# Kernel tuning notes

Hardware: AMD Instinct MI355X
Metric: run time of the kernel (lower is better)

Reference implementation:

```python
import jax, jax.numpy as jnp
import numpy as np

N = 4096          # n_nodes
M = 8192          # m_nodes (= 2*N, required by block structure)
D = 128           # in_dim == hidden_dim (conv1 is reapplied to its own output)
H = 128
NUM_ITERS = 3


def setup_inputs() -> dict:
    key = jax.random.key(0)
    ks = jax.random.split(key, 6)
    X = jax.random.normal(ks[0], (N, D), dtype=jnp.float32)
    R = jax.random.uniform(ks[1], (N, N), dtype=jnp.float32)
    A = 0.5 * (R + R.T)  # symmetric, strictly positive connectivity matrix
    # upsample MLP: Linear(n_nodes -> m_nodes - n_nodes), torch weight layout [out, in]
    W_up = jax.random.normal(ks[2], (M - N, N), dtype=jnp.float32) * 0.02
    b_up = jnp.zeros((M - N,), dtype=jnp.float32)
    # GCNConv linear weights stored [in, out]
    W1 = jax.random.normal(ks[3], (D, H), dtype=jnp.float32) * 0.05
    b1 = jnp.zeros((H,), dtype=jnp.float32)
    W2 = jax.random.normal(ks[4], (H, H), dtype=jnp.float32) * 0.05
    b2 = jnp.zeros((H,), dtype=jnp.float32)
    return dict(X=X, A=A, W_up=W_up, b_up=b_up, W1=W1, b1=b1, W2=W2, b2=b2)


def _gcn(Adj, X, W, b):
    # PyG GCNConv on a fully dense, strictly-positive weighted graph:
    # every diagonal entry is nonzero, so add_remaining_self_loops is a no-op and
    # out = D^{-1/2} A D^{-1/2} (X W) + b  exactly.
    deg = Adj.sum(axis=0)                         # [m] column degree
    dinv = jnp.where(deg > 0, jax.lax.rsqrt(deg), 0.0)
    An = Adj * dinv[:, None] * dinv[None, :]      # symmetric normalization
    return An @ (X @ W) + b


def reference(X, A, W_up, b_up, W1, b1, W2, b2):
    # new_nodes = upsample_mlp(X.T).T  -> [M-N, D]
    new_nodes = (X.T @ W_up.T + b_up).T
    Xu = jnp.concatenate([X, new_nodes], axis=0)  # [M, D]
    # block adjacency: [[A, A.T], [A, sigmoid(new @ new.T)]]
    Adj = jnp.block([[A, A.T],
                     [A, jax.nn.sigmoid(new_nodes @ new_nodes.T)]])  # [M, M]
    A_out = Adj
    for _ in range(NUM_ITERS):
        Xu = jax.nn.relu(_gcn(Adj, Xu, W1, b1))
        Adj = jax.nn.sigmoid(Xu @ Xu.T)           # mid-loop adjacency rebuild
        Xu = jax.nn.relu(_gcn(Adj, Xu, W2, b2))
        A_out = jax.nn.sigmoid(Xu @ Xu.T)
        # NOTE: edge_index for the next conv1 is NOT rebuilt from A_out in the
        # original (only after conv1), so Adj carries the mid-loop matrix.
    return A_out
```

## Files before the change

kernel.cpp:

```cpp
#include <hip/hip_runtime.h>
#include <hip/hip_bf16.h>


#define N_NODES 4096
#define M_NODES 8192
#define DIM 128
#define SLICE_ELEMS ((size_t)M_NODES * DIM)

typedef __attribute__((ext_vector_type(4))) float f32x4;
typedef __attribute__((ext_vector_type(8))) short bf16x8;

__device__ __forceinline__ unsigned short f2bf(float f) {
  union { float f; unsigned u; } v; v.f = f;
  unsigned r = v.u + 0x7fffu + ((v.u >> 16) & 1u);
  return (unsigned short)(r >> 16);
}

__device__ __forceinline__ void gld16(unsigned short* lds, const unsigned short* g) {
  __builtin_amdgcn_global_load_lds(
      (const __attribute__((address_space(1))) unsigned int*)g,
      (__attribute__((address_space(3))) unsigned int*)lds, 16, 0, 0);
}

__device__ __forceinline__ float sigmoidf_(float x) { return 1.0f / (1.0f + __expf(-x)); }


__global__ void cast_x_kernel(const float* __restrict__ X, unsigned short* __restrict__ Xu,
                              unsigned short* __restrict__ XT,
                              float* __restrict__ colsumA) {
  int idx = blockIdx.x * 256 + threadIdx.x;
  if (idx < N_NODES) colsumA[idx] = 0.f;
  int i = idx >> 7, c = idx & 127;
  unsigned short b = f2bf(X[idx]);
  Xu[idx] = b;
  XT[(size_t)c * N_NODES + i] = b;
}

__global__ void cast_wt2_kernel(const float* __restrict__ W1, const float* __restrict__ W2,
                                unsigned short* __restrict__ WT1,
                                unsigned short* __restrict__ WT2) {
  int idx = blockIdx.x * 256 + threadIdx.x;
  const float* W = idx < 16384 ? W1 : W2;
  unsigned short* WT = idx < 16384 ? WT1 : WT2;
  int j = idx & 16383;
  int k = j >> 7, c = j & 127;
  WT[c * DIM + k] = f2bf(W[j]);
}

__global__ void cast_a_kernel(const float* __restrict__ A, unsigned short* __restrict__ Adj,
                              float* __restrict__ colsumA) {
  int c = blockIdx.x * 256 + threadIdx.x;
  int r0 = blockIdx.y * 128;
  int tm = r0 >> 7;
  int kc = c >> 10, st = (c & 1023) >> 5, e = c & 31;
  size_t a1 = ((size_t)(tm)      * 8 + kc)     * 131072 + (size_t)st * 4096 + e;
  size_t a2 = ((size_t)(tm)      * 8 + 4 + kc) * 131072 + (size_t)st * 4096 + e;
  size_t a3 = ((size_t)(tm + 32) * 8 + kc)     * 131072 + (size_t)st * 4096 + e;
  float s = 0.f;
  for (int r = 0; r < 128; ++r) {
    float a = A[(size_t)(r0 + r) * N_NODES + c];
    unsigned short b = f2bf(a);
    Adj[a1 + r * 32] = b; Adj[a2 + r * 32] = b; Adj[a3 + r * 32] = b;
    s += a;
  }
  atomicAdd(&colsumA[c], s);
}

__global__ void init_deg_kernel(const float* __restrict__ colsumA, float* __restrict__ deg) {
  int i = blockIdx.x * 256 + threadIdx.x;
  deg[i] = (i < N_NODES) ? 2.0f * colsumA[i] : colsumA[i - N_NODES];
}


__global__ __launch_bounds__(256, 2)
void agg128_kernel(const unsigned short* __restrict__ At,
                   const unsigned short* __restrict__ BT, long ldb,
                   float* __restrict__ accBase, int kIters) {
  __shared__ __align__(16) unsigned short smem[32768];
  const int t = threadIdx.x, w = t >> 6, lane = t & 63;
  const int q = lane >> 4, l15 = lane & 15;
  const int xk = l15 & 7;
  const int tm = blockIdx.x;
  const int sg0 = blockIdx.y * (kIters * 2);
  const size_t kbase = (size_t)sg0 * 32;

  auto STAGE = [&](int s, int b) {
    unsigned short* la = smem + b * 16384;
    unsigned short* lb = la + 8192;
#pragma unroll
    for (int j = 0; j < 4; ++j) {
      int ch = j * 256 + t;
      int row = ch >> 3, phys = ch & 7;
      int c = phys ^ (row & 7);
      int sg = sg0 + 2 * s + (c >> 2);
      gld16(&la[ch * 8],
            &At[((size_t)tm * 8 + (sg >> 5)) * 131072 + (size_t)(sg & 31) * 4096 +
                row * 32 + (c & 3) * 8]);
      gld16(&lb[ch * 8], &BT[(size_t)row * ldb + kbase + s * 64 + c * 8]);
    }
  };

  f32x4 acc[2][8];
#pragma unroll
  for (int a = 0; a < 2; ++a)
#pragma unroll
    for (int b = 0; b < 8; ++b) acc[a][b] = (f32x4)0.f;

  STAGE(0, 0);

  for (int s = 0; s < kIters; ++s) {
    if (s + 1 < kIters) {
      STAGE(s + 1, (s + 1) & 1);
      asm volatile("s_waitcnt vmcnt(8)" ::: "memory");
    } else {
      asm volatile("s_waitcnt vmcnt(0)" ::: "memory");
    }
    __builtin_amdgcn_s_barrier();
    __builtin_amdgcn_sched_barrier(0);

    const unsigned short* la = smem + (s & 1) * 16384;
    const unsigned short* lb = la + 8192;
#pragma unroll
    for (int kk = 0; kk < 2; ++kk) {
      bf16x8 a0 = *(const bf16x8*)&la[(w * 32 + l15) * 64 + (((kk << 2) + q) ^ xk) * 8];
      bf16x8 a1 = *(const bf16x8*)&la[(w * 32 + 16 + l15) * 64 + (((kk << 2) + q) ^ xk) * 8];
#pragma unroll
      for (int nt = 0; nt < 8; ++nt) {
        bf16x8 b = *(const bf16x8*)&lb[(nt * 16 + l15) * 64 + (((kk << 2) + q) ^ xk) * 8];
        acc[0][nt] = __builtin_amdgcn_mfma_f32_16x16x32_bf16(a0, b, acc[0][nt], 0, 0, 0);
        acc[1][nt] = __builtin_amdgcn_mfma_f32_16x16x32_bf16(a1, b, acc[1][nt], 0, 0, 0);
      }
    }
    __builtin_amdgcn_sched_barrier(0);
    __builtin_amdgcn_s_barrier();
    __builtin_amdgcn_sched_barrier(0);
  }
  float* ct = accBase + (size_t)blockIdx.y * SLICE_ELEMS + (size_t)blockIdx.x * 16384;
#pragma unroll
  for (int mt = 0; mt < 2; ++mt)
#pragma unroll
    for (int nt = 0; nt < 8; ++nt)
      *(f32x4*)&ct[((w * 16 + mt * 8 + nt) * 256) + (q * 16 + l15) * 4] = acc[mt][nt];
}


__global__ __launch_bounds__(256)
void up_agg_f32(const float* __restrict__ Wup, const unsigned short* __restrict__ BT,
                float* __restrict__ accBase) {
  __shared__ __align__(16) unsigned short smem[6144];
  unsigned short* la = smem;
  unsigned short* lb = smem + 2048;
  const int t = threadIdx.x, w = t >> 6, lane = t & 63;
  const int q = lane >> 4, l15 = lane & 15;
  const int r0 = blockIdx.x * 64;
  const int k0 = blockIdx.y * 512;
  const int arow = t >> 2, achk = t & 3;

  f32x4 acc[8];
#pragma unroll
  for (int b = 0; b < 8; ++b) acc[b] = (f32x4)0.f;

  for (int s = 0; s < 16; ++s) {
    int kb = k0 + s * 32;
    __syncthreads();
    gld16(&lb[t * 8],        &BT[(size_t)arow * N_NODES + kb + achk * 8]);
    gld16(&lb[2048 + t * 8], &BT[(size_t)(64 + arow) * N_NODES + kb + achk * 8]);
    const float* ap = &Wup[(size_t)(r0 + (t >> 2)) * N_NODES + kb + (t & 3) * 8];
    float4 v0 = *(const float4*)ap;
    float4 v1 = *(const float4*)(ap + 4);
    ushort4 o0, o1;
    o0.x = f2bf(v0.x); o0.y = f2bf(v0.y); o0.z = f2bf(v0.z); o0.w = f2bf(v0.w);
    o1.x = f2bf(v1.x); o1.y = f2bf(v1.y); o1.z = f2bf(v1.z); o1.w = f2bf(v1.w);
    *(ushort4*)&la[t * 8] = o0;
    *(ushort4*)&la[t * 8 + 4] = o1;
    __syncthreads();

    bf16x8 a0 = *(const bf16x8*)&la[(w * 16 + l15) * 32 + q * 8];
#pragma unroll
    for (int nt = 0; nt < 8; ++nt) {
      bf16x8 b = *(const bf16x8*)&lb[(nt * 16 + l15) * 32 + q * 8];
      acc[nt] = __builtin_amdgcn_mfma_f32_16x16x32_bf16(a0, b, acc[nt], 0, 0, 0);
    }
  }
  float* ct = accBase + (size_t)blockIdx.y * SLICE_ELEMS + (size_t)blockIdx.x * 8192;
#pragma unroll
  for (int nt = 0; nt < 8; ++nt)
    *(f32x4*)&ct[((w * 8 + nt) * 256) + (q * 16 + l15) * 4] = acc[nt];
}

__global__ void reduce64_kernel(const float* __restrict__ acc,
                                unsigned short* __restrict__ dst,
                                const float* __restrict__ bias_row,
                                const float* __restrict__ bias_col,
                                const float* __restrict__ deg, int mode, int nSlices) {
  int p = blockIdx.x * 256 + threadIdx.x;
  float s = 0.f;
  for (int sp = 0; sp < nSlices; ++sp) s += acc[(size_t)sp * SLICE_ELEMS + p];
  int row, col;
  float v;
  if (mode == 0) {
    int tile = p >> 13, r = p & 8191;
    int grp = r >> 8;
    int w = grp >> 3, nt = grp & 7;
    int r2 = r & 255;
    int i = r2 & 3, ql = r2 >> 2;
    row = tile * 64 + w * 16 + (ql >> 4) * 4 + i;
    col = nt * 16 + (ql & 15);
    v = s + bias_row[row];
  } else {
    int tile = p >> 14, r = p & 16383;
    int grp = r >> 8;
    int w = grp >> 4, mt = (grp >> 3) & 1, nt = grp & 7;
    int r2 = r & 255;
    int i = r2 & 3, ql = r2 >> 2;
    row = tile * 128 + w * 32 + mt * 16 + (ql >> 4) * 4 + i;
    col = nt * 16 + (ql & 15);
    float d = deg[row];
    float dv = d > 0.f ? rsqrtf(d) : 0.f;
    v = fmaxf(dv * s + bias_col[col], 0.f);
  }
  dst[(size_t)row * DIM + col] = f2bf(v);
}


template <int MODE>
__global__ __launch_bounds__(256)
void rebuild_kernel(const unsigned short* __restrict__ XA,
                    const unsigned short* __restrict__ XB,
                    void* __restrict__ out, long p1 ,
                    long col0, float* __restrict__ deg, int nB) {
  __shared__ __align__(16) unsigned short smem[34816];
  __shared__ float lcol[128];
  __shared__ float lrow[128];
  unsigned short* lA = smem;
  unsigned short* lB = smem + 16384;
  const int t = threadIdx.x, w = t >> 6, lane = t & 63;
  const int q = lane >> 4, l15 = lane & 15;
  const int sx = (l15 >> 1) & 3;

  int rem = blockIdx.x, bi = 0;
  while (rem >= nB - bi) { rem -= nB - bi; ++bi; }
  const int bj = bi + rem;
  const int i0 = bi * 128, j0 = bj * 128;
  const bool offdiag = (bi != bj);

  const int srow = t >> 2;
  const int xchk = (t & 3) ^ ((t >> 3) & 3);
#pragma unroll
  for (int kk = 0; kk < 4; ++kk)
#pragma unroll
    for (int h = 0; h < 2; ++h) {
      gld16(&lA[kk * 4096 + h * 2048 + t * 8],
            &XA[(size_t)(i0 + h * 64 + srow) * DIM + kk * 32 + xchk * 8]);
      gld16(&lB[kk * 4096 + h * 2048 + t * 8],
            &XB[(size_t)(j0 + h * 64 + srow) * DIM + kk * 32 + xchk * 8]);
    }
  if (MODE == 0 && t < 128) { lcol[t] = 0.f; lrow[t] = 0.f; }
  __syncthreads();

  f32x4 acc[2][8];
#pragma unroll
  for (int a = 0; a < 2; ++a)
#pragma unroll
    for (int b = 0; b < 8; ++b) acc[a][b] = (f32x4)0.f;

#pragma unroll
  for (int kk = 0; kk < 4; ++kk) {
    bf16x8 a0 = *(const bf16x8*)&lA[kk * 4096 + (w * 32 + l15) * 32 + ((q ^ sx)) * 8];
    bf16x8 a1 = *(const bf16x8*)&lA[kk * 4096 + (w * 32 + 16 + l15) * 32 + ((q ^ sx)) * 8];
#pragma unroll
    for (int nt = 0; nt < 8; ++nt) {
      bf16x8 b = *(const bf16x8*)&lB[kk * 4096 + (nt * 16 + l15) * 32 + ((q ^ sx)) * 8];
      acc[0][nt] = __builtin_amdgcn_mfma_f32_16x16x32_bf16(a0, b, acc[0][nt], 0, 0, 0);
      acc[1][nt] = __builtin_amdgcn_mfma_f32_16x16x32_bf16(a1, b, acc[1][nt], 0, 0, 0);
    }
  }
  __syncthreads();

  if (MODE == 0) {
    unsigned short* lC  = smem;
    unsigned short* lCt = smem + 17408;
    float rs[2][4] = {{0.f, 0.f, 0.f, 0.f}, {0.f, 0.f, 0.f, 0.f}};
#pragma unroll
    for (int mt = 0; mt < 2; ++mt)
#pragma unroll
      for (int nt = 0; nt < 8; ++nt) {
        float cs = 0.f;
#pragma unroll
        for (int i = 0; i < 4; ++i) {
          float sv = sigmoidf_(acc[mt][nt][i]);
          cs += sv;
          unsigned short hb = f2bf(sv);
          int row = w * 32 + mt * 16 + q * 4 + i, colL = nt * 16 + l15;
          lC[row * 136 + colL] = hb;
          if (offdiag) { lCt[colL * 136 + row] = hb; rs[mt][i] += sv; }
        }
        cs += __shfl_xor(cs, 16);
        cs += __shfl_xor(cs, 32);
        if (lane < 16) atomicAdd(&lcol[nt * 16 + lane], cs);
      }
    if (offdiag) {
#pragma unroll
      for (int mt = 0; mt < 2; ++mt)
#pragma unroll
        for (int i = 0; i < 4; ++i) {
          float v = rs[mt][i];
          v += __shfl_xor(v, 1); v += __shfl_xor(v, 2);
          v += __shfl_xor(v, 4); v += __shfl_xor(v, 8);
          if (l15 == 0) atomicAdd(&lrow[w * 32 + mt * 16 + q * 4 + i], v);
        }
    }
    __syncthreads();
    unsigned short* og = (unsigned short*)out;
    {
      const long rowbase = p1 + i0, colbase = col0 + j0;
      const size_t tb = ((size_t)(rowbase >> 7) * 8 + (colbase >> 10)) * 131072;
      const int stb = (int)((colbase & 1023) >> 5);
#pragma unroll
      for (int cc = 0; cc < 8; ++cc) {
        int ch = t + cc * 256;
        int row = ch >> 4, c16 = ch & 15;
        *(bf16x8*)&og[tb + (size_t)(stb + (c16 >> 2)) * 4096 + row * 32 + (c16 & 3) * 8] =
            *(const bf16x8*)&lC[row * 136 + c16 * 8];
      }
    }
    if (offdiag) {
      const long rowbase = p1 + j0, colbase = col0 + i0;
      const size_t tb = ((size_t)(rowbase >> 7) * 8 + (colbase >> 10)) * 131072;
      const int stb = (int)((colbase & 1023) >> 5);
#pragma unroll
      for (int cc = 0; cc < 8; ++cc) {
        int ch = t + cc * 256;
        int row = ch >> 4, c16 = ch & 15;
        *(bf16x8*)&og[tb + (size_t)(stb + (c16 >> 2)) * 4096 + row * 32 + (c16 & 3) * 8] =
            *(const bf16x8*)&lCt[row * 136 + c16 * 8];
      }
    }
    if (t < 128) atomicAdd(&deg[col0 + j0 + t], lcol[t]);
    if (offdiag && t < 128) atomicAdd(&deg[col0 + i0 + t], lrow[t]);
  } else {
    float* og = (float*)out;
    float* lCf = (float*)smem;
#pragma unroll
    for (int mt = 0; mt < 2; ++mt)
#pragma unroll
      for (int nt = 0; nt < 8; ++nt)
#pragma unroll
        for (int i = 0; i < 4; ++i) acc[mt][nt][i] = sigmoidf_(acc[mt][nt][i]);
#pragma unroll
    for (int h2 = 0; h2 < 2; ++h2) {
      __syncthreads();
      if ((w >> 1) == h2) {
#pragma unroll
        for (int mt = 0; mt < 2; ++mt)
#pragma unroll
          for (int nt = 0; nt < 8; ++nt)
#pragma unroll
            for (int i = 0; i < 4; ++i)
              lCf[((w & 1) * 32 + mt * 16 + q * 4 + i) * 132 + nt * 16 + l15] =
                  acc[mt][nt][i];
      }
      __syncthreads();
#pragma unroll
      for (int j = 0; j < 8; ++j) {
        int ch = t + j * 256;
        int r64 = ch >> 5, c4 = (ch & 31) * 4;
        *(f32x4*)&og[(size_t)(i0 + h2 * 64 + r64) * p1 + j0 + c4] =
            *(const f32x4*)&lCf[r64 * 132 + c4];
      }
    }
    if (offdiag) {
#pragma unroll
      for (int h2 = 0; h2 < 2; ++h2) {
        __syncthreads();
#pragma unroll
        for (int mt = 0; mt < 2; ++mt)
#pragma unroll
          for (int nt = 0; nt < 8; ++nt)
            if ((nt >> 2) == h2) {
#pragma unroll
              for (int i = 0; i < 4; ++i)
                lCf[((nt & 3) * 16 + l15) * 132 + (w * 32 + mt * 16 + q * 4 + i)] =
                    acc[mt][nt][i];
            }
        __syncthreads();
#pragma unroll
        for (int j = 0; j < 8; ++j) {
          int ch = t + j * 256;
          int r64 = ch >> 5, c4 = (ch & 31) * 4;
          *(f32x4*)&og[(size_t)(j0 + h2 * 64 + r64) * p1 + i0 + c4] =
              *(const f32x4*)&lCf[r64 * 132 + c4];
        }
      }
    }
  }
}


__global__ __launch_bounds__(256)
void yz_kernel(const unsigned short* __restrict__ Xu, const unsigned short* __restrict__ WT,
               const float* __restrict__ deg, unsigned short* __restrict__ ZT, int ldz,
               float* __restrict__ zbuf) {
  __shared__ __align__(16) unsigned short smem[32768];
  unsigned short* lA = smem;
  unsigned short* lB = smem + 16384;
  const int t = threadIdx.x, w = t >> 6, lane = t & 63;
  const int q = lane >> 4, l15 = lane & 15;
  const int sx = (l15 >> 1) & 3;
  const int r0 = blockIdx.x * 128;
  if (zbuf) {
    int gid = blockIdx.x * 256 + t;
    if (gid < M_NODES) zbuf[gid] = 0.f;
  }
  const int srow = t >> 2;
  const int xchk = (t & 3) ^ ((t >> 3) & 3);
#pragma unroll
  for (int kk = 0; kk < 4; ++kk)
#pragma unroll
    for (int h = 0; h < 2; ++h) {
      gld16(&lA[kk * 4096 + h * 2048 + t * 8],
            &Xu[(size_t)(r0 + h * 64 + srow) * DIM + kk * 32 + xchk * 8]);
      gld16(&lB[kk * 4096 + h * 2048 + t * 8],
            &WT[(size_t)(h * 64 + srow) * DIM + kk * 32 + xchk * 8]);
    }
  __syncthreads();

  f32x4 acc[2][8];
#pragma unroll
  for (int a = 0; a < 2; ++a)
#pragma unroll
    for (int b = 0; b < 8; ++b) acc[a][b] = (f32x4)0.f;

#pragma unroll
  for (int kk = 0; kk < 4; ++kk) {
    bf16x8 a0 = *(const bf16x8*)&lA[kk * 4096 + (w * 32 + l15) * 32 + (q ^ sx) * 8];
    bf16x8 a1 = *(const bf16x8*)&lA[kk * 4096 + (w * 32 + 16 + l15) * 32 + (q ^ sx) * 8];
#pragma unroll
    for (int nt = 0; nt < 8; ++nt) {
      bf16x8 b = *(const bf16x8*)&lB[kk * 4096 + (nt * 16 + l15) * 32 + (q ^ sx) * 8];
      acc[0][nt] = __builtin_amdgcn_mfma_f32_16x16x32_bf16(a0, b, acc[0][nt], 0, 0, 0);
      acc[1][nt] = __builtin_amdgcn_mfma_f32_16x16x32_bf16(a1, b, acc[1][nt], 0, 0, 0);
    }
  }
  __syncthreads();
  unsigned short* lT = smem;
#pragma unroll
  for (int mt = 0; mt < 2; ++mt)
#pragma unroll
    for (int i = 0; i < 4; ++i) {
      int r = w * 32 + mt * 16 + q * 4 + i;
      float d = deg[r0 + r];
      float dv = d > 0.f ? rsqrtf(d) : 0.f;
#pragma unroll
      for (int nt = 0; nt < 8; ++nt)
        lT[(nt * 16 + l15) * 136 + r] = f2bf(dv * acc[mt][nt][i]);
    }
  __syncthreads();
#pragma unroll
  for (int cc = 0; cc < 8; ++cc) {
    int ch = t + cc * 256;
    int c = ch >> 4, c16 = ch & 15;
    *(bf16x8*)&ZT[(size_t)c * ldz + r0 + c16 * 8] = *(const bf16x8*)&lT[c * 136 + c16 * 8];
  }
}


extern "C" void kernel_launch(void* const* d_in, const int* in_sizes, int n_in,
                              void* d_out, int out_size, void* d_ws, size_t ws_size,
                              hipStream_t stream) {
  (void)in_sizes; (void)n_in; (void)out_size;
  const float* X   = (const float*)d_in[0];
  const float* A   = (const float*)d_in[1];
  const float* Wup = (const float*)d_in[2];
  const float* bup = (const float*)d_in[3];
  const float* W1  = (const float*)d_in[4];
  const float* b1  = (const float*)d_in[5];
  const float* W2  = (const float*)d_in[6];
  const float* b2  = (const float*)d_in[7];

  const size_t ADJ_BYTES = (size_t)M_NODES * M_NODES * 2;
  char* ws = (char*)d_ws;
  size_t off = 0;
  auto alloc = [&](size_t bytes) {
    char* p = ws + off;
    off += (bytes + 255) & ~(size_t)255;
    return p;
  };
  float*          accb    = (float*)alloc(8 * SLICE_ELEMS * 4);
  unsigned short* Xu      = (unsigned short*)alloc((size_t)M_NODES * DIM * 2);
  unsigned short* ZT      = (unsigned short*)alloc((size_t)DIM * M_NODES * 2);
  unsigned short* XT      = (unsigned short*)alloc((size_t)DIM * N_NODES * 2);
  unsigned short* W1T     = (unsigned short*)alloc(DIM * DIM * 2);
  unsigned short* W2T     = (unsigned short*)alloc(DIM * DIM * 2);
  float*          colsumA = (float*)alloc(N_NODES * 4);
  float*          degA    = (float*)alloc(M_NODES * 4);
  float*          degB    = (float*)alloc(M_NODES * 4);

  unsigned short* Adj;
  if (ws_size >= off + ADJ_BYTES) Adj = (unsigned short*)(ws + off);
  else                            Adj = (unsigned short*)d_out;

  unsigned short* XuNew = Xu + (size_t)N_NODES * DIM;

  cast_x_kernel<<<N_NODES * DIM / 256, 256, 0, stream>>>(X, Xu, XT, colsumA);
  cast_wt2_kernel<<<128, 256, 0, stream>>>(W1, W2, W1T, W2T);

  up_agg_f32<<<dim3(N_NODES / 64, 8), 256, 0, stream>>>(Wup, XT, accb);
  reduce64_kernel<<<N_NODES * DIM / 256, 256, 0, stream>>>(
      accb, XuNew, bup, nullptr, nullptr, 0, 8);

  cast_a_kernel<<<dim3(N_NODES / 256, N_NODES / 128), 256, 0, stream>>>(A, Adj, colsumA);
  init_deg_kernel<<<M_NODES / 256, 256, 0, stream>>>(colsumA, degA);
  rebuild_kernel<0><<<32 * 33 / 2, 256, 0, stream>>>(
      XuNew, XuNew, Adj, N_NODES, N_NODES, degA, 32);

  float* degCur = degA;
  float* degMid = degB;
  for (int it = 0; it < 3; ++it) {
    yz_kernel<<<M_NODES / 128, 256, 0, stream>>>(Xu, W1T, degCur, ZT, M_NODES, degMid);
    agg128_kernel<<<dim3(M_NODES / 128, 8), 256, 0, stream>>>(Adj, ZT, M_NODES, accb, 16);
    reduce64_kernel<<<M_NODES * DIM / 256, 256, 0, stream>>>(
        accb, Xu, nullptr, b1, degCur, 1, 8);
    rebuild_kernel<0><<<64 * 65 / 2, 256, 0, stream>>>(
        Xu, Xu, Adj, 0, 0, degMid, 64);
    yz_kernel<<<M_NODES / 128, 256, 0, stream>>>(Xu, W2T, degMid, ZT, M_NODES, nullptr);
    agg128_kernel<<<dim3(M_NODES / 128, 8), 256, 0, stream>>>(Adj, ZT, M_NODES, accb, 16);
    reduce64_kernel<<<M_NODES * DIM / 256, 256, 0, stream>>>(
        accb, Xu, nullptr, b2, degMid, 1, 8);
    if (it == 2)
      rebuild_kernel<1><<<64 * 65 / 2, 256, 0, stream>>>(
          Xu, Xu, d_out, M_NODES, 0, nullptr, 64);
    float* tmp = degCur; degCur = degMid; degMid = tmp;
  }
}
```

Before: 905.2 us.

## Fuse split-K reduction into agg128 via last-block atomic counter

```diff
diff --git a/kernel.cpp b/kernel.cpp
--- a/kernel.cpp
+++ b/kernel.cpp
@@ -27,9 +27,10 @@
 
 __global__ void cast_x_kernel(const float* __restrict__ X, unsigned short* __restrict__ Xu,
                               unsigned short* __restrict__ XT,
-                              float* __restrict__ colsumA) {
+                              float* __restrict__ colsumA, unsigned* __restrict__ cnts) {
   int idx = blockIdx.x * 256 + threadIdx.x;
   if (idx < N_NODES) colsumA[idx] = 0.f;
+  if (idx < 384) cnts[idx] = 0u;
   int i = idx >> 7, c = idx & 127;
   unsigned short b = f2bf(X[idx]);
   Xu[idx] = b;
@@ -75,7 +76,9 @@
 __global__ __launch_bounds__(256, 2)
 void agg128_kernel(const unsigned short* __restrict__ At,
                    const unsigned short* __restrict__ BT, long ldb,
-                   float* __restrict__ accBase, int kIters) {
+                   float* __restrict__ accBase, int kIters,
+                   unsigned* __restrict__ cnt, unsigned short* __restrict__ dst,
+                   const float* __restrict__ bias_col, const float* __restrict__ deg) {
   __shared__ __align__(16) unsigned short smem[32768];
   const int t = threadIdx.x, w = t >> 6, lane = t & 63;
   const int q = lane >> 4, l15 = lane & 15;
@@ -135,12 +138,44 @@
     __builtin_amdgcn_s_barrier();
     __builtin_amdgcn_sched_barrier(0);
   }
-  float* ct = accBase + (size_t)blockIdx.y * SLICE_ELEMS + (size_t)blockIdx.x * 16384;
+  float* ct = accBase + (size_t)blockIdx.y * SLICE_ELEMS + (size_t)tm * 16384;
 #pragma unroll
   for (int mt = 0; mt < 2; ++mt)
 #pragma unroll
     for (int nt = 0; nt < 8; ++nt)
       *(f32x4*)&ct[((w * 16 + mt * 8 + nt) * 256) + (q * 16 + l15) * 4] = acc[mt][nt];
+
+  __shared__ int lastFlag;
+  if (t == 0) {
+    __threadfence();
+    unsigned old = atomicAdd(&cnt[tm], 1u);
+    lastFlag = (old == 7u);
+  }
+  __syncthreads();
+  if (!lastFlag) return;
+  __threadfence();
+  const float* __restrict__ base = accBase + (size_t)tm * 16384;
+#pragma unroll 4
+  for (int j = 0; j < 16; ++j) {
+    int p4 = j * 256 + t;
+    f32x4 sum = (f32x4)0.f;
+#pragma unroll
+    for (int sp = 0; sp < 8; ++sp)
+      sum += *(const f32x4*)&base[(size_t)sp * SLICE_ELEMS + (size_t)p4 * 4];
+    int p = p4 * 4;
+    int grp = p >> 8;
+    int ww = grp >> 4, mt = (grp >> 3) & 1, nt = grp & 7;
+    int ql = (p & 255) >> 2;
+    int row0 = tm * 128 + ww * 32 + mt * 16 + (ql >> 4) * 4;
+    int col = nt * 16 + (ql & 15);
+    float bc = bias_col[col];
+#pragma unroll
+    for (int i = 0; i < 4; ++i) {
+      float d = deg[row0 + i];
+      float dv = d > 0.f ? rsqrtf(d) : 0.f;
+      dst[(size_t)(row0 + i) * DIM + col] = f2bf(fmaxf(dv * sum[i] + bc, 0.f));
+    }
+  }
 }
 
 
@@ -190,36 +225,18 @@
 
 __global__ void reduce64_kernel(const float* __restrict__ acc,
                                 unsigned short* __restrict__ dst,
-                                const float* __restrict__ bias_row,
-                                const float* __restrict__ bias_col,
-                                const float* __restrict__ deg, int mode, int nSlices) {
+                                const float* __restrict__ bias_row, int nSlices) {
   int p = blockIdx.x * 256 + threadIdx.x;
   float s = 0.f;
   for (int sp = 0; sp < nSlices; ++sp) s += acc[(size_t)sp * SLICE_ELEMS + p];
-  int row, col;
-  float v;
-  if (mode == 0) {
-    int tile = p >> 13, r = p & 8191;
-    int grp = r >> 8;
-    int w = grp >> 3, nt = grp & 7;
-    int r2 = r & 255;
-    int i = r2 & 3, ql = r2 >> 2;
-    row = tile * 64 + w * 16 + (ql >> 4) * 4 + i;
-    col = nt * 16 + (ql & 15);
-    v = s + bias_row[row];
-  } else {
-    int tile = p >> 14, r = p & 16383;
-    int grp = r >> 8;
-    int w = grp >> 4, mt = (grp >> 3) & 1, nt = grp & 7;
-    int r2 = r & 255;
-    int i = r2 & 3, ql = r2 >> 2;
-    row = tile * 128 + w * 32 + mt * 16 + (ql >> 4) * 4 + i;
-    col = nt * 16 + (ql & 15);
-    float d = deg[row];
-    float dv = d > 0.f ? rsqrtf(d) : 0.f;
-    v = fmaxf(dv * s + bias_col[col], 0.f);
-  }
-  dst[(size_t)row * DIM + col] = f2bf(v);
+  int tile = p >> 13, r = p & 8191;
+  int grp = r >> 8;
+  int w = grp >> 3, nt = grp & 7;
+  int r2 = r & 255;
+  int i = r2 & 3, ql = r2 >> 2;
+  int row = tile * 64 + w * 16 + (ql >> 4) * 4 + i;
+  int col = nt * 16 + (ql & 15);
+  dst[(size_t)row * DIM + col] = f2bf(s + bias_row[row]);
 }
 
 
@@ -495,6 +512,7 @@
   float*          colsumA = (float*)alloc(N_NODES * 4);
   float*          degA    = (float*)alloc(M_NODES * 4);
   float*          degB    = (float*)alloc(M_NODES * 4);
+  unsigned*       cnts    = (unsigned*)alloc(6 * 64 * 4);
 
   unsigned short* Adj;
   if (ws_size >= off + ADJ_BYTES) Adj = (unsigned short*)(ws + off);
@@ -502,12 +520,11 @@
 
   unsigned short* XuNew = Xu + (size_t)N_NODES * DIM;
 
-  cast_x_kernel<<<N_NODES * DIM / 256, 256, 0, stream>>>(X, Xu, XT, colsumA);
+  cast_x_kernel<<<N_NODES * DIM / 256, 256, 0, stream>>>(X, Xu, XT, colsumA, cnts);
   cast_wt2_kernel<<<128, 256, 0, stream>>>(W1, W2, W1T, W2T);
 
   up_agg_f32<<<dim3(N_NODES / 64, 8), 256, 0, stream>>>(Wup, XT, accb);
-  reduce64_kernel<<<N_NODES * DIM / 256, 256, 0, stream>>>(
-      accb, XuNew, bup, nullptr, nullptr, 0, 8);
+  reduce64_kernel<<<N_NODES * DIM / 256, 256, 0, stream>>>(accb, XuNew, bup, 8);
 
   cast_a_kernel<<<dim3(N_NODES / 256, N_NODES / 128), 256, 0, stream>>>(A, Adj, colsumA);
   init_deg_kernel<<<M_NODES / 256, 256, 0, stream>>>(colsumA, degA);
@@ -516,17 +533,18 @@
 
   float* degCur = degA;
   float* degMid = degB;
+  int call = 0;
   for (int it = 0; it < 3; ++it) {
     yz_kernel<<<M_NODES / 128, 256, 0, stream>>>(Xu, W1T, degCur, ZT, M_NODES, degMid);
-    agg128_kernel<<<dim3(M_NODES / 128, 8), 256, 0, stream>>>(Adj, ZT, M_NODES, accb, 16);
-    reduce64_kernel<<<M_NODES * DIM / 256, 256, 0, stream>>>(
-        accb, Xu, nullptr, b1, degCur, 1, 8);
+    agg128_kernel<<<dim3(M_NODES / 128, 8), 256, 0, stream>>>(
+        Adj, ZT, M_NODES, accb, 16, cnts + 64 * call, Xu, b1, degCur);
+    ++call;
     rebuild_kernel<0><<<64 * 65 / 2, 256, 0, stream>>>(
         Xu, Xu, Adj, 0, 0, degMid, 64);
     yz_kernel<<<M_NODES / 128, 256, 0, stream>>>(Xu, W2T, degMid, ZT, M_NODES, nullptr);
-    agg128_kernel<<<dim3(M_NODES / 128, 8), 256, 0, stream>>>(Adj, ZT, M_NODES, accb, 16);
-    reduce64_kernel<<<M_NODES * DIM / 256, 256, 0, stream>>>(
-        accb, Xu, nullptr, b2, degMid, 1, 8);
+    agg128_kernel<<<dim3(M_NODES / 128, 8), 256, 0, stream>>>(
+        Adj, ZT, M_NODES, accb, 16, cnts + 64 * call, Xu, b2, degMid);
+    ++call;
     if (it == 2)
       rebuild_kernel<1><<<64 * 65 / 2, 256, 0, stream>>>(
           Xu, Xu, d_out, M_NODES, 0, nullptr, 64);
```

Result: slower. 1.049 ms (+15.9%).
